# Performance work log

Hardware: AMD Instinct MI355X
Metric: run time of the kernel (lower is better)

The kernel has to match this reference:

```python
import jax, jax.numpy as jnp
import numpy as np

T, B, S = 128, 128, 128
H, E, V, L = 1024, 512, 32000, 2


def setup_inputs() -> dict:
    key = jax.random.key(0)
    ks = jax.random.split(key, 16)
    s = 0.02
    inp = {
        "inputs": jax.random.randint(ks[0], (T, B), 0, V),
        "h0": jax.random.normal(ks[1], (L, B, H), jnp.float32) * 0.1,
        "c0": jax.random.normal(ks[2], (L, B, H), jnp.float32) * 0.1,
        "contexts": jax.random.normal(ks[3], (B, S, H), jnp.float32),
        "emb": jax.random.normal(ks[4], (V, E), jnp.float32) * s,
        "W_ih0": jax.random.normal(ks[5], (4 * H, E), jnp.float32) * s,
        "W_hh0": jax.random.normal(ks[6], (4 * H, H), jnp.float32) * s,
        "b_ih0": jnp.zeros((4 * H,), jnp.float32),
        "b_hh0": jnp.zeros((4 * H,), jnp.float32),
        "W_ih1": jax.random.normal(ks[7], (4 * H, H), jnp.float32) * s,
        "W_hh1": jax.random.normal(ks[8], (4 * H, H), jnp.float32) * s,
        "b_ih1": jnp.zeros((4 * H,), jnp.float32),
        "b_hh1": jnp.zeros((4 * H,), jnp.float32),
        "att_in_W": jax.random.normal(ks[9], (H, H), jnp.float32) * s,
        "att_in_b": jnp.zeros((H,), jnp.float32),
        "att_out_W": jax.random.normal(ks[10], (H, 2 * H), jnp.float32) * s,
        "att_out_b": jnp.zeros((H,), jnp.float32),
    }
    return inp


def _lstm_cell(x, h, c, Wih, Whh, bih, bhh):
    # torch.nn.LSTMCell: gates in (i, f, g, o) order
    gates = x @ Wih.T + bih + h @ Whh.T + bhh  # [B, 4H]
    i, f, g, o = jnp.split(gates, 4, axis=-1)
    c2 = jax.nn.sigmoid(f) * c + jax.nn.sigmoid(i) * jnp.tanh(g)
    h2 = jax.nn.sigmoid(o) * jnp.tanh(c2)
    return h2, c2


def reference(inputs, h0, c0, contexts, emb,
              W_ih0, W_hh0, b_ih0, b_hh0,
              W_ih1, W_hh1, b_ih1, b_hh1,
              att_in_W, att_in_b, att_out_W, att_out_b):
    layer_params = [(W_ih0, W_hh0, b_ih0, b_hh0), (W_ih1, W_hh1, b_ih1, b_hh1)]
    embs = emb[inputs]  # [T, B, E]

    def step(carry, x_t):
        h, c = carry  # each [L, B, H]
        x = x_t
        hs, cs = [], []
        for l, (Wih, Whh, bih, bhh) in enumerate(layer_params):
            h_l, c_l = _lstm_cell(x, h[l], c[l], Wih, Whh, bih, bhh)
            x = h_l  # dropout=0.0 / eval mode -> identity
            hs.append(h_l)
            cs.append(c_l)
        # global (Luong general) attention
        gamma = x @ att_in_W.T + att_in_b                     # [B, H]
        scores = jnp.einsum('bsh,bh->bs', contexts, gamma)    # [B, S]
        w = jax.nn.softmax(scores, axis=-1)
        c_t = jnp.einsum('bs,bsh->bh', w, contexts)           # [B, H]
        out = jnp.tanh(jnp.concatenate([c_t, x], axis=-1) @ att_out_W.T + att_out_b)
        return (jnp.stack(hs), jnp.stack(cs)), (out, w)

    (hT, cT), (outputs, attns) = jax.lax.scan(step, (h0, c0), embs)
    return outputs, hT, cT
```

## Files before the change

### kernel.cpp

```cpp
#include <hip/hip_runtime.h>

#define TT 128
#define BB 128
#define SS 128
#define HH 1024
#define EE 512
#define BH (BB*HH)

typedef unsigned short u16;
typedef unsigned long long u64;
typedef __attribute__((ext_vector_type(8))) short s8v;
typedef __attribute__((ext_vector_type(4))) float f32x4;

__device__ __forceinline__ float b2f(u16 u) {
    union { unsigned int i; float f; } v; v.i = ((unsigned int)u) << 16; return v.f;
}
__device__ __forceinline__ u16 f2b(float f) {
    union { float f; unsigned int i; } v; v.f = f;
    unsigned int x = v.i;
    x = x + 0x7fffu + ((x >> 16) & 1u);
    return (u16)(x >> 16);
}
__device__ __forceinline__ float sigm(float x) {
    float t = __expf(-fabsf(x));
    float p = 1.0f / (1.0f + t);
    return x >= 0.0f ? p : 1.0f - p;
}
__device__ __forceinline__ float tanh_(float x) {
    float t = __expf(-2.0f * fabsf(x));
    float r = (1.0f - t) / (1.0f + t);
    return x >= 0.0f ? r : -r;
}

#define MFMA(a, b, c) __builtin_amdgcn_mfma_f32_16x16x32_bf16((a), (b), (c), 0, 0, 0)

__global__ __launch_bounds__(256)
void cvt_k(const float* __restrict__ s, u16* __restrict__ d, int n)
{
    const int i = (blockIdx.x * 256 + threadIdx.x) * 4;
    if (i < n) {
        const float4 v = *(const float4*)(s + i);
        ushort4 o;
        o.x = f2b(v.x); o.y = f2b(v.y); o.z = f2b(v.z); o.w = f2b(v.w);
        *(ushort4*)(d + i) = o;
    }
}

__global__ __launch_bounds__(128)
void gather_k(const int* __restrict__ toks, const float* __restrict__ emb,
              u16* __restrict__ X)
{
    const int row = blockIdx.x;
    const int tok = toks[row];
    const int c = threadIdx.x * 4;
    const float4 v = *(const float4*)(emb + (size_t)tok * EE + c);
    ushort4 o;
    o.x = f2b(v.x); o.y = f2b(v.y); o.z = f2b(v.z); o.w = f2b(v.w);
    *(ushort4*)(X + (size_t)row * EE + c) = o;
}

__global__ __launch_bounds__(256)
void init_k(const float* __restrict__ h0in,
            u16* __restrict__ h0ring, u16* __restrict__ h1init,
            int* __restrict__ barcnt)
{
    const int i = blockIdx.x * 256 + threadIdx.x;
    const u16 hb = f2b(h0in[i]);
    if (i < BH) h0ring[i] = hb;
    else        h1init[i - BH] = hb;
    if (i < 512) barcnt[i] = 0;
}

__global__ __launch_bounds__(512, 1)
void scan_k(const float* __restrict__ Wih0, const float* __restrict__ Whh0,
            const float* __restrict__ Wih1, const float* __restrict__ Whh1,
            const float* __restrict__ bih0, const float* __restrict__ bhh0,
            const float* __restrict__ bih1, const float* __restrict__ bhh1,
            const float* __restrict__ c0in,
            const u16* __restrict__ Xb,
            u16* __restrict__ h0ring,
            const u16* __restrict__ h1init,
            u16* __restrict__ H1all,
            float* __restrict__ outT,
            int* __restrict__ barcnt)
{
    extern __shared__ u16 lds[];
    u16* W0x = lds;
    u16* W0h = W0x + 16*4*16*8;
    u16* W1x = W0h + 32*4*16*8;
    u16* W1h = W1x + 32*4*16*8;
    float* gst0 = (float*)(W1h + 32*4*16*8);
    float* gst1 = gst0 + 8*16*20;

    const int tid  = threadIdx.x;
    const int bk   = blockIdx.x;
    const int j0   = (((bk & 7) << 5) | (bk >> 3)) * 4;
    const int lane = tid & 63;
    const int w    = tid >> 6;
    const int l15  = lane & 15, quad = lane >> 4;

    int* barA = barcnt;
    int* barB = barcnt + 256;

    auto loadW = [&](const float* src, int K, u16* dst) {
        const int ntup = (K / 32) * 4 * 16;
        for (int idx = tid; idx < ntup; idx += 512) {
            const int n = idx & 15, q = (idx >> 4) & 3, kc = idx >> 6;
            const int col = ((n >> 2) * HH) + j0 + (n & 3);
            const float* sp = src + (size_t)col * K + kc * 32 + q * 8;
            const float4 v0 = *(const float4*)(sp);
            const float4 v1 = *(const float4*)(sp + 4);
            u16* dp = dst + (size_t)idx * 8;
            dp[0] = f2b(v0.x); dp[1] = f2b(v0.y); dp[2] = f2b(v0.z); dp[3] = f2b(v0.w);
            dp[4] = f2b(v1.x); dp[5] = f2b(v1.y); dp[6] = f2b(v1.z); dp[7] = f2b(v1.w);
        }
    };
    loadW(Wih0, EE, W0x);
    loadW(Whh0, HH, W0h);
    loadW(Wih1, HH, W1x);
    loadW(Whh1, HH, W1h);

    const int pr = tid & 127;
    f32x4 cst = (f32x4)0.0f;
    f32x4 bs0 = (f32x4)0.0f, bs1 = (f32x4)0.0f, bs2 = (f32x4)0.0f, bs3 = (f32x4)0.0f;
    if (tid < 256) {
        const int layer = tid >> 7;
        const float* bi = layer ? bih1 : bih0;
        const float* bh = layer ? bhh1 : bhh0;
        cst = *(const f32x4*)(c0in + (size_t)layer * BH + (size_t)pr * HH + j0);
        bs0 = *(const f32x4*)(bi + 0 * HH + j0) + *(const f32x4*)(bh + 0 * HH + j0);
        bs1 = *(const f32x4*)(bi + 1 * HH + j0) + *(const f32x4*)(bh + 1 * HH + j0);
        bs2 = *(const f32x4*)(bi + 2 * HH + j0) + *(const f32x4*)(bh + 2 * HH + j0);
        bs3 = *(const f32x4*)(bi + 3 * HH + j0) + *(const f32x4*)(bh + 3 * HH + j0);
    }

    __syncthreads();

    const int arow = w * 16 + l15;

    #define BIDX(kc) (((size_t)((kc) * 4 + quad) * 16 + l15) * 8)

    auto pointwise = [&](const float* gbase, u16* dst, float* oH, float* oC,
                         bool doOut) {
        const float* gr = gbase + (pr >> 4) * 320 + (pr & 15) * 20;
        const f32x4 vi = *(const f32x4*)(gr + 0);
        const f32x4 vf = *(const f32x4*)(gr + 4);
        const f32x4 vg = *(const f32x4*)(gr + 8);
        const f32x4 vo = *(const f32x4*)(gr + 12);
        f32x4 hv;
        #pragma unroll
        for (int jj = 0; jj < 4; ++jj) {
            const float gi = vi[jj] + bs0[jj];
            const float gf = vf[jj] + bs1[jj];
            const float gg = vg[jj] + bs2[jj];
            const float go = vo[jj] + bs3[jj];
            const float c = sigm(gf) * cst[jj] + sigm(gi) * tanh_(gg);
            cst[jj] = c;
            hv[jj] = sigm(go) * tanh_(c);
        }
        const u64 pk = (u64)f2b(hv[0]) | ((u64)f2b(hv[1]) << 16)
                     | ((u64)f2b(hv[2]) << 32) | ((u64)f2b(hv[3]) << 48);
        __hip_atomic_store((u64*)(dst + (size_t)pr * HH + j0), pk,
                           __ATOMIC_RELAXED, __HIP_MEMORY_SCOPE_AGENT);
        if (doOut) {
            *(f32x4*)(oH + (size_t)pr * HH + j0) = hv;
            *(f32x4*)(oC + (size_t)pr * HH + j0) = cst;
        }
    };

    for (int p = 0; p <= TT; ++p) {
        f32x4 acc0 = (f32x4)0.0f, acc1 = (f32x4)0.0f;

        if (p < TT) {
            const u16* ap = Xb + ((size_t)p * BB + arow) * EE + quad * 8;
            #pragma unroll 8
            for (int kc = 0; kc < 16; ++kc) {
                s8v a = *(const s8v*)(ap + kc * 32);
                acc0 = MFMA(a, *(const s8v*)(W0x + BIDX(kc)), acc0);
            }
        }

        if (p > 0) {
            if (tid < 8) {
                const int target = 32 * p;
                while (__hip_atomic_load(barA + tid * 32, __ATOMIC_RELAXED,
                                         __HIP_MEMORY_SCOPE_AGENT) < target) {
                    __builtin_amdgcn_s_sleep(1);
                }
            }
            __syncthreads();
            asm volatile("" ::: "memory");
        }

        {
            const u16* a0p = h0ring + (size_t)p * BH + (size_t)arow * HH + quad * 8;
            if (p < TT) {
                #pragma unroll 8
                for (int kc = 0; kc < 32; ++kc) {
                    s8v a0 = *(const s8v*)(a0p + kc * 32);
                    acc0 = MFMA(a0, *(const s8v*)(W0h + BIDX(kc)), acc0);
                    acc1 = MFMA(a0, *(const s8v*)(W1x + BIDX(kc)), acc1);
                }
            } else {
                #pragma unroll 8
                for (int kc = 0; kc < 32; ++kc) {
                    s8v a0 = *(const s8v*)(a0p + kc * 32);
                    acc1 = MFMA(a0, *(const s8v*)(W1x + BIDX(kc)), acc1);
                }
            }
        }

        if (p < TT) {
            #pragma unroll
            for (int r = 0; r < 4; ++r)
                gst0[w * 320 + (quad * 4 + r) * 20 + l15] = acc0[r];
        }
        __syncthreads();
        if (p < TT && tid < 128)
            pointwise(gst0, h0ring + (size_t)(p + 1) * BH,
                      outT + (size_t)0 * BH, outT + (size_t)2 * BH, p == TT - 1);
        if (p >= 2 && tid >= 256 && tid < 264) {
            const int target = 32 * (p - 1);
            while (__hip_atomic_load(barB + (tid - 256) * 32, __ATOMIC_RELAXED,
                                     __HIP_MEMORY_SCOPE_AGENT) < target) {
                __builtin_amdgcn_s_sleep(1);
            }
        }
        __syncthreads();
        asm volatile("" ::: "memory");
        if (p < TT && tid == 0)
            __hip_atomic_fetch_add(barA + (bk & 7) * 32, 1, __ATOMIC_RELAXED,
                                   __HIP_MEMORY_SCOPE_AGENT);

        if (p > 0) {
            const u16* h1p = (p == 1) ? h1init : (H1all + (size_t)(p - 2) * BH);
            const u16* a1p = h1p + (size_t)arow * HH + quad * 8;
            #pragma unroll 8
            for (int kc = 0; kc < 32; ++kc) {
                s8v a1 = *(const s8v*)(a1p + kc * 32);
                acc1 = MFMA(a1, *(const s8v*)(W1h + BIDX(kc)), acc1);
            }
            #pragma unroll
            for (int r = 0; r < 4; ++r)
                gst1[w * 320 + (quad * 4 + r) * 20 + l15] = acc1[r];
        }
        __syncthreads();
        if (p > 0 && tid >= 128 && tid < 256)
            pointwise(gst1, H1all + (size_t)(p - 1) * BH,
                      outT + (size_t)1 * BH, outT + (size_t)3 * BH, p == TT);
        __syncthreads();
        if (p > 0 && tid == 0)
            __hip_atomic_fetch_add(barB + (bk & 7) * 32, 1, __ATOMIC_RELAXED,
                                   __HIP_MEMORY_SCOPE_AGENT);
    }
    #undef BIDX
}

__global__ __launch_bounds__(256)
void gemm_bt_k(const u16* __restrict__ A1, int K1,
               const u16* __restrict__ A2, int K2,
               const u16* __restrict__ W, int ldw,
               const float* __restrict__ bias,
               u16* __restrict__ Cb, float* __restrict__ Cf,
               int N, int act)
{
    const int lane = threadIdx.x & 63;
    const int wave = threadIdx.x >> 6;
    const int l15 = lane & 15, quad = lane >> 4;
    const int n0 = blockIdx.x * 64;
    const int mrow = blockIdx.y * 64 + wave * 16;
    const int arow = mrow + l15;

    f32x4 acc[4];
    #pragma unroll
    for (int nt = 0; nt < 4; ++nt) acc[nt] = (f32x4)0.0f;

    const u16* wr0 = W + (size_t)(n0 + 0 * 16 + l15) * ldw + quad * 8;
    const u16* wr1 = W + (size_t)(n0 + 1 * 16 + l15) * ldw + quad * 8;
    const u16* wr2 = W + (size_t)(n0 + 2 * 16 + l15) * ldw + quad * 8;
    const u16* wr3 = W + (size_t)(n0 + 3 * 16 + l15) * ldw + quad * 8;

    {
        const u16* ap = A1 + (size_t)arow * K1 + quad * 8;
        #pragma unroll 4
        for (int kk = 0; kk < K1; kk += 32) {
            s8v a = *(const s8v*)(ap + kk);
            acc[0] = MFMA(a, *(const s8v*)(wr0 + kk), acc[0]);
            acc[1] = MFMA(a, *(const s8v*)(wr1 + kk), acc[1]);
            acc[2] = MFMA(a, *(const s8v*)(wr2 + kk), acc[2]);
            acc[3] = MFMA(a, *(const s8v*)(wr3 + kk), acc[3]);
        }
    }
    if (A2 != nullptr) {
        const u16* ap = A2 + (size_t)arow * K2 + quad * 8;
        #pragma unroll 4
        for (int kk = 0; kk < K2; kk += 32) {
            s8v a = *(const s8v*)(ap + kk);
            acc[0] = MFMA(a, *(const s8v*)(wr0 + K1 + kk), acc[0]);
            acc[1] = MFMA(a, *(const s8v*)(wr1 + K1 + kk), acc[1]);
            acc[2] = MFMA(a, *(const s8v*)(wr2 + K1 + kk), acc[2]);
            acc[3] = MFMA(a, *(const s8v*)(wr3 + K1 + kk), acc[3]);
        }
    }
    #pragma unroll
    for (int nt = 0; nt < 4; ++nt) {
        const int col = n0 + nt * 16 + l15;
        const float bv = bias[col];
        #pragma unroll
        for (int r = 0; r < 4; ++r) {
            const int row = mrow + quad * 4 + r;
            float v = acc[nt][r] + bv;
            if (act) v = tanh_(v);
            if (Cf) Cf[(size_t)row * N + col] = v;
            else    Cb[(size_t)row * N + col] = f2b(v);
        }
    }
}

__global__ __launch_bounds__(256)
void attn_k(const u16* __restrict__ gamma, const float* __restrict__ ctx,
            u16* __restrict__ ctall)
{
    const int b = blockIdx.x;
    const int t0 = blockIdx.y * 16;
    const int tid = threadIdx.x;
    const int lane = tid & 63, wave = tid >> 6;
    const int l15 = lane & 15, quad = lane >> 4;

    __shared__ float sw[16 * SS];

    {
        f32x4 acc0 = (f32x4)0.0f, acc1 = (f32x4)0.0f;
        const u16*   ap  = gamma + ((size_t)(t0 + l15) * BB + b) * HH + quad * 8;
        const float* bp0 = ctx + ((size_t)b * SS + (wave * 32 + l15)) * HH + quad * 8;
        const float* bp1 = ctx + ((size_t)b * SS + (wave * 32 + 16 + l15)) * HH + quad * 8;
        for (int kk = 0; kk < HH; kk += 32) {
            s8v a = *(const s8v*)(ap + kk);
            float4 u0 = *(const float4*)(bp0 + kk);
            float4 u1 = *(const float4*)(bp0 + kk + 4);
            s8v bv;
            bv[0] = (short)f2b(u0.x); bv[1] = (short)f2b(u0.y);
            bv[2] = (short)f2b(u0.z); bv[3] = (short)f2b(u0.w);
            bv[4] = (short)f2b(u1.x); bv[5] = (short)f2b(u1.y);
            bv[6] = (short)f2b(u1.z); bv[7] = (short)f2b(u1.w);
            acc0 = MFMA(a, bv, acc0);
            float4 w0 = *(const float4*)(bp1 + kk);
            float4 w1 = *(const float4*)(bp1 + kk + 4);
            s8v cv;
            cv[0] = (short)f2b(w0.x); cv[1] = (short)f2b(w0.y);
            cv[2] = (short)f2b(w0.z); cv[3] = (short)f2b(w0.w);
            cv[4] = (short)f2b(w1.x); cv[5] = (short)f2b(w1.y);
            cv[6] = (short)f2b(w1.z); cv[7] = (short)f2b(w1.w);
            acc1 = MFMA(a, cv, acc1);
        }
        #pragma unroll
        for (int r = 0; r < 4; ++r) {
            const int trow = quad * 4 + r;
            sw[trow * SS + wave * 32 + l15] = acc0[r];
            sw[trow * SS + wave * 32 + 16 + l15] = acc1[r];
        }
    }
    __syncthreads();

    {
        const int row = tid >> 4, c0 = tid & 15;
        float e[8];
        float m = -1e30f;
        #pragma unroll
        for (int k = 0; k < 8; ++k) { e[k] = sw[row * SS + c0 + k * 16]; m = fmaxf(m, e[k]); }
        #pragma unroll
        for (int off = 8; off >= 1; off >>= 1) m = fmaxf(m, __shfl_xor(m, off));
        float s = 0.0f;
        #pragma unroll
        for (int k = 0; k < 8; ++k) { e[k] = __expf(e[k] - m); s += e[k]; }
        #pragma unroll
        for (int off = 8; off >= 1; off >>= 1) s += __shfl_xor(s, off);
        const float inv = 1.0f / s;
        #pragma unroll
        for (int k = 0; k < 8; ++k) sw[row * SS + c0 + k * 16] = e[k] * inv;
    }
    __syncthreads();

    {
        const int h0 = tid * 4;
        float a[16][4];
        #pragma unroll
        for (int t = 0; t < 16; ++t)
            #pragma unroll
            for (int q = 0; q < 4; ++q) a[t][q] = 0.0f;

        const float* cp = ctx + (size_t)b * SS * HH + h0;
        for (int s = 0; s < SS; ++s) {
            const float4 cv = *(const float4*)(cp + (size_t)s * HH);
            #pragma unroll
            for (int t = 0; t < 16; ++t) {
                const float wgt = sw[t * SS + s];
                a[t][0] += wgt * cv.x;
                a[t][1] += wgt * cv.y;
                a[t][2] += wgt * cv.z;
                a[t][3] += wgt * cv.w;
            }
        }
        #pragma unroll
        for (int t = 0; t < 16; ++t) {
            u16* op = ctall + ((size_t)(t0 + t) * BB + b) * HH + h0;
            #pragma unroll
            for (int q = 0; q < 4; ++q) op[q] = f2b(a[t][q]);
        }
    }
}

extern "C" void kernel_launch(void* const* d_in, const int* in_sizes, int n_in,
                              void* d_out, int out_size, void* d_ws, size_t ws_size,
                              hipStream_t stream)
{
    const int*   toks = (const int*)d_in[0];
    const float* h0in = (const float*)d_in[1];
    const float* c0in = (const float*)d_in[2];
    const float* ctx  = (const float*)d_in[3];
    const float* emb  = (const float*)d_in[4];
    const float* Wih0 = (const float*)d_in[5];
    const float* Whh0 = (const float*)d_in[6];
    const float* bih0 = (const float*)d_in[7];
    const float* bhh0 = (const float*)d_in[8];
    const float* Wih1 = (const float*)d_in[9];
    const float* Whh1 = (const float*)d_in[10];
    const float* bih1 = (const float*)d_in[11];
    const float* bhh1 = (const float*)d_in[12];
    const float* attW = (const float*)d_in[13];
    const float* attb = (const float*)d_in[14];
    const float* outW = (const float*)d_in[15];
    const float* outb = (const float*)d_in[16];

    u16*   h0ring = (u16*)d_ws;
    u16*   h1init = h0ring + (size_t)(TT + 1) * BH;
    int*   barcnt = (int*)(h1init + BH);
    u16*   Xb     = (u16*)(barcnt + 512);
    u16*   H1all  = Xb + (size_t)TT * BB * EE;
    u16*   gammaA = H1all + (size_t)TT * BH;
    u16*   attWb  = gammaA + (size_t)TT * BH;
    u16*   outWb  = attWb + (size_t)HH * HH;
    u16*   ctall  = h0ring;

    cvt_k<<<dim3((HH * HH / 4 + 255) / 256), 256, 0, stream>>>(attW, attWb, HH * HH);
    cvt_k<<<dim3((2 * HH * HH / 4 + 255) / 256), 256, 0, stream>>>(outW, outWb, 2 * HH * HH);

    gather_k<<<dim3(TT * BB), 128, 0, stream>>>(toks, emb, Xb);
    init_k<<<dim3(2 * BH / 256), 256, 0, stream>>>(h0in, h0ring, h1init, barcnt);

    float* outp = (float*)d_out;
    const int ldsBytes = (16*4*16*8 + 3 * 32*4*16*8) * 2 + 2 * 8*16*20 * 4;
    hipFuncSetAttribute((const void*)scan_k,
                        hipFuncAttributeMaxDynamicSharedMemorySize, ldsBytes);
    scan_k<<<dim3(256), 512, ldsBytes, stream>>>(
        Wih0, Whh0, Wih1, Whh1, bih0, bhh0, bih1, bhh1, c0in,
        Xb, h0ring, h1init, H1all, outp + (size_t)TT * BH, barcnt);

    gemm_bt_k<<<dim3(HH / 64, (TT * BB) / 64), 256, 0, stream>>>(
        H1all, HH, nullptr, 0, attWb, HH, attb, gammaA, nullptr, HH, 0);

    attn_k<<<dim3(BB, TT / 16), 256, 0, stream>>>(gammaA, ctx, ctall);

    gemm_bt_k<<<dim3(HH / 64, (TT * BB) / 64), 256, 0, stream>>>(
        ctall, HH, H1all, HH, outWb, 2 * HH, outb, nullptr, outp, HH, 1);
}
```

Measured before the change: 3.841 ms.

## Re-skew LSTM layer wavefront so layer-1 work hides layer-0 barrier wait

Restructures the persistent two-layer LSTM loop so layer 1 lags layer 0 by two steps instead of one. In each iteration, layer-1 work (its W1x product on the previous layer-0 output, its recurrent product and pointwise update) runs before the block waits on the layer-0 grid barrier, then the layer-0 recurrent GEMM and pointwise run. The goal is to take the cross-block barrier wait off the critical path of the layer-0 recurrence. The cost is one extra loop iteration, reordered synchronisation with more __syncthreads, and a longer spin sleep interval that may add polling latency.

```diff
diff --git a/kernel.cpp b/kernel.cpp
--- a/kernel.cpp
+++ b/kernel.cpp
@@ -168,10 +168,21 @@
         }
     };
 
-    for (int p = 0; p <= TT; ++p) {
+    auto poll = [&](int* bar, int target) {
+        if (tid < 8) {
+            while (__hip_atomic_load(bar + tid * 32, __ATOMIC_RELAXED,
+                                     __HIP_MEMORY_SCOPE_AGENT) < target) {
+                __builtin_amdgcn_s_sleep(4);
+            }
+        }
+    };
+
+    for (int p = 0; p <= TT + 1; ++p) {
+        const bool L0 = (p < TT);
+        const bool L1 = (p >= 2);
         f32x4 acc0 = (f32x4)0.0f, acc1 = (f32x4)0.0f;
 
-        if (p < TT) {
+        if (L0) {
             const u16* ap = Xb + ((size_t)p * BB + arow) * EE + quad * 8;
             #pragma unroll 8
             for (int kc = 0; kc < 16; ++kc) {
@@ -180,60 +191,22 @@
             }
         }
 
-        if (p > 0) {
-            if (tid < 8) {
-                const int target = 32 * p;
-                while (__hip_atomic_load(barA + tid * 32, __ATOMIC_RELAXED,
-                                         __HIP_MEMORY_SCOPE_AGENT) < target) {
-                    __builtin_amdgcn_s_sleep(1);
-                }
-            }
-            __syncthreads();
-            asm volatile("" ::: "memory");
-        }
-
-        {
-            const u16* a0p = h0ring + (size_t)p * BH + (size_t)arow * HH + quad * 8;
-            if (p < TT) {
-                #pragma unroll 8
-                for (int kc = 0; kc < 32; ++kc) {
-                    s8v a0 = *(const s8v*)(a0p + kc * 32);
-                    acc0 = MFMA(a0, *(const s8v*)(W0h + BIDX(kc)), acc0);
-                    acc1 = MFMA(a0, *(const s8v*)(W1x + BIDX(kc)), acc1);
-                }
-            } else {
-                #pragma unroll 8
-                for (int kc = 0; kc < 32; ++kc) {
-                    s8v a0 = *(const s8v*)(a0p + kc * 32);
-                    acc1 = MFMA(a0, *(const s8v*)(W1x + BIDX(kc)), acc1);
-                }
-            }
-        }
-
-        if (p < TT) {
-            #pragma unroll
-            for (int r = 0; r < 4; ++r)
-                gst0[w * 320 + (quad * 4 + r) * 20 + l15] = acc0[r];
-        }
-        __syncthreads();
-        if (p < TT && tid < 128)
-            pointwise(gst0, h0ring + (size_t)(p + 1) * BH,
-                      outT + (size_t)0 * BH, outT + (size_t)2 * BH, p == TT - 1);
-        if (p >= 2 && tid >= 256 && tid < 264) {
-            const int target = 32 * (p - 1);
-            while (__hip_atomic_load(barB + (tid - 256) * 32, __ATOMIC_RELAXED,
-                                     __HIP_MEMORY_SCOPE_AGENT) < target) {
-                __builtin_amdgcn_s_sleep(1);
-            }
-        }
+        if (L1) {
+            const u16* a0p = h0ring + (size_t)(p - 1) * BH
+                           + (size_t)arow * HH + quad * 8;
+            #pragma unroll 8
+            for (int kc = 0; kc < 32; ++kc) {
+                s8v a0 = *(const s8v*)(a0p + kc * 32);
+                acc1 = MFMA(a0, *(const s8v*)(W1x + BIDX(kc)), acc1);
+            }
+        }
+
+        if (p >= 3) poll(barB, 32 * (p - 2));
         __syncthreads();
         asm volatile("" ::: "memory");
-        if (p < TT && tid == 0)
-            __hip_atomic_fetch_add(barA + (bk & 7) * 32, 1, __ATOMIC_RELAXED,
-                                   __HIP_MEMORY_SCOPE_AGENT);
-
-        if (p > 0) {
-            const u16* h1p = (p == 1) ? h1init : (H1all + (size_t)(p - 2) * BH);
+
+        if (L1) {
+            const u16* h1p = (p == 2) ? h1init : (H1all + (size_t)(p - 3) * BH);
             const u16* a1p = h1p + (size_t)arow * HH + quad * 8;
             #pragma unroll 8
             for (int kc = 0; kc < 32; ++kc) {
@@ -245,12 +218,37 @@
                 gst1[w * 320 + (quad * 4 + r) * 20 + l15] = acc1[r];
         }
         __syncthreads();
-        if (p > 0 && tid >= 128 && tid < 256)
-            pointwise(gst1, H1all + (size_t)(p - 1) * BH,
-                      outT + (size_t)1 * BH, outT + (size_t)3 * BH, p == TT);
-        __syncthreads();
-        if (p > 0 && tid == 0)
+        if (L1 && tid >= 128 && tid < 256)
+            pointwise(gst1, H1all + (size_t)(p - 2) * BH,
+                      outT + (size_t)1 * BH, outT + (size_t)3 * BH, p == TT + 1);
+        __syncthreads();
+        if (L1 && tid == 0)
             __hip_atomic_fetch_add(barB + (bk & 7) * 32, 1, __ATOMIC_RELAXED,
+                                   __HIP_MEMORY_SCOPE_AGENT);
+
+        if (p >= 1 && p <= TT) poll(barA, 32 * p);
+        __syncthreads();
+        asm volatile("" ::: "memory");
+
+        if (L0) {
+            const u16* a0p = h0ring + (size_t)p * BH
+                           + (size_t)arow * HH + quad * 8;
+            #pragma unroll 8
+            for (int kc = 0; kc < 32; ++kc) {
+                s8v a0 = *(const s8v*)(a0p + kc * 32);
+                acc0 = MFMA(a0, *(const s8v*)(W0h + BIDX(kc)), acc0);
+            }
+            #pragma unroll
+            for (int r = 0; r < 4; ++r)
+                gst0[w * 320 + (quad * 4 + r) * 20 + l15] = acc0[r];
+        }
+        __syncthreads();
+        if (L0 && tid < 128)
+            pointwise(gst0, h0ring + (size_t)(p + 1) * BH,
+                      outT + (size_t)0 * BH, outT + (size_t)2 * BH, p == TT - 1);
+        __syncthreads();
+        if (L0 && tid == 0)
+            __hip_atomic_fetch_add(barA + (bk & 7) * 32, 1, __ATOMIC_RELAXED,
                                    __HIP_MEMORY_SCOPE_AGENT);
     }
     #undef BIDX
```

Result: slower. 4.808 ms (+25.2%).
